# Kernel optimization log

Measured on AMD Instinct MI355X. Metric: run time of the kernel, lower is better.

Reference implementation:

```python
import jax, jax.numpy as jnp
import numpy as np

NQ, NH = 7, 4          # quantiles x horizons
G = NQ * NH            # 28 independent branches
IN_DIM, H1, H2 = 64, 64, 32


def setup_inputs() -> dict:
    key = jax.random.key(0)
    ks = jax.random.split(key, 7)
    B = 131072
    x = jax.random.normal(ks[0], (B, IN_DIM), dtype=jnp.float32)
    s1 = 1.0 / np.sqrt(IN_DIM)
    s2 = 1.0 / np.sqrt(H1)
    s3 = 1.0 / np.sqrt(H2)
    W1 = jax.random.uniform(ks[1], (G, IN_DIM, H1), jnp.float32, -s1, s1)
    b1 = jax.random.uniform(ks[2], (G, H1), jnp.float32, -s1, s1)
    W2 = jax.random.uniform(ks[3], (G, H1, H2), jnp.float32, -s2, s2)
    b2 = jax.random.uniform(ks[4], (G, H2), jnp.float32, -s2, s2)
    W3 = jax.random.uniform(ks[5], (G, H2, 1), jnp.float32, -s3, s3)
    b3 = jax.random.uniform(ks[6], (G, 1), jnp.float32, -s3, s3)
    return {"x": x, "W1": W1, "b1": b1, "W2": W2, "b2": b2, "W3": W3, "b3": b3}


def reference(x, W1, b1, W2, b2, W3, b3):
    # All G branches fused as batched GEMMs. x: [B, in]
    B = x.shape[0]
    h = jax.nn.relu(jnp.einsum('bi,gij->gbj', x, W1) + b1[:, None, :])   # [G,B,H1]
    h = jax.nn.relu(jnp.einsum('gbj,gjk->gbk', h, W2) + b2[:, None, :])  # [G,B,H2]
    o = jnp.einsum('gbk,gko->gbo', h, W3) + b3[:, None, :]               # [G,B,1]
    # branch order matches nested loop: quantile outer, horizon inner
    out = o[..., 0].reshape(NQ, NH, B).transpose(2, 0, 1)                # [B,NQ,NH]
    return out
```

## Files before the change

kernel.cpp:

```cpp
#include <hip/hip_runtime.h>
#include <hip/hip_bf16.h>
#include <hip/hip_fp16.h>

#define GN 28
#define G_TILE_BYTES 12288
#define WS_BYTES (GN * G_TILE_BYTES)

typedef __attribute__((ext_vector_type(4))) float f32x4;
typedef __attribute__((ext_vector_type(8))) short short8;
typedef _Float16 f16x8 __attribute__((ext_vector_type(8)));

__device__ __forceinline__ unsigned short f2h(float v){
  __half h = __float2half(v);
  return __builtin_bit_cast(unsigned short, h);
}
__device__ __forceinline__ f32x4 mfma16f(short8 a, short8 b, f32x4 c){
  return __builtin_amdgcn_mfma_f32_16x16x32_f16(
      __builtin_bit_cast(f16x8, a), __builtin_bit_cast(f16x8, b), c, 0, 0, 0);
}

__global__ void split_weights(const float* __restrict__ W1,
                              const float* __restrict__ W2,
                              unsigned char* __restrict__ ws){
  int t = blockIdx.x * 256 + threadIdx.x;
  if (t < 57344){
    int g = t >> 11, rem = t & 2047, n = rem >> 5, m = rem & 31;
    float v0 = W1[(g*64 + 2*m    )*64 + n];
    float v1 = W1[(g*64 + 2*m + 1)*64 + n];
    int off = (n*128 + 4*m) ^ ((n & 7) << 4);
    unsigned char* base = ws + g*G_TILE_BYTES;
    *(unsigned int*)(base + off) = (unsigned)f2h(v0) | ((unsigned)f2h(v1) << 16);
  } else {
    int t2 = t - 57344;
    int g = t2 >> 10, rem = t2 & 1023, n2 = rem >> 5, m = rem & 31;
    int kk = 2*m;
    int ks = kk >> 5, qq = (kk >> 3) & 3, u = (kk >> 2) & 1, i = kk & 3;
    int kn = 32*ks + 16*u + 4*qq + i;
    float v0 = W2[(g*64 + kn    )*32 + n2];
    float v1 = W2[(g*64 + kn + 1)*32 + n2];
    int off = (n2*128 + 4*m) ^ ((n2 & 7) << 4);
    unsigned char* base = ws + g*G_TILE_BYTES + 8192;
    *(unsigned int*)(base + off) = (unsigned)f2h(v0) | ((unsigned)f2h(v1) << 16);
  }
}

__global__ __launch_bounds__(256, 2) void mlp_fused(
    const float* __restrict__ x,  const float* __restrict__ b1,
    const float* __restrict__ b2, const float* __restrict__ W3,
    const float* __restrict__ b3, const unsigned char* __restrict__ ws,
    float* __restrict__ out){
  __shared__ uint4 wbuf[2][768];
  __shared__ float outb[256*28];
  __shared__ float biasL[3616];

  const int tid = threadIdx.x;
  const int wv  = tid >> 6;
  const int ln  = tid & 63;
  const int l15 = ln & 15;
  const int q   = ln >> 4;
  const int rowBase = blockIdx.x * 256 + wv * 64;

  #pragma unroll
  for (int i = 0; i < 7; ++i) biasL[i*256 + tid] = b1[i*256 + tid];
  if (tid < 128){
    #pragma unroll
    for (int i = 0; i < 7; ++i){
      biasL[1792 + i*128 + tid] = b2[i*128 + tid];
      biasL[2688 + i*128 + tid] = W3[i*128 + tid];
    }
  }
  if (tid < 28) biasL[3584 + tid] = b3[tid];

  short8 xf[4][2];
  #pragma unroll
  for (int rt = 0; rt < 4; ++rt)
    #pragma unroll
    for (int ks = 0; ks < 2; ++ks){
      const float* p = x + (rowBase + rt*16 + l15)*64 + ks*32 + q*8;
      f32x4 a = *(const f32x4*)p;
      f32x4 b = *(const f32x4*)(p + 4);
      short8 s;
      #pragma unroll
      for (int j = 0; j < 4; ++j){
        s[j]   = (short)f2h(a[j]);
        s[4+j] = (short)f2h(b[j]);
      }
      xf[rt][ks] = s;
    }

  auto stage = [&](int g, int buf){
    const unsigned char* gb = ws + g*G_TILE_BYTES + wv*3072 + ln*16;
    uint4* lb = &wbuf[buf][wv*192];
    #pragma unroll
    for (int it = 0; it < 3; ++it){
      __builtin_amdgcn_global_load_lds(
          (const __attribute__((address_space(1))) void*)(gb + it*1024),
          (__attribute__((address_space(3))) void*)(lb + it*64), 16, 0, 0);
    }
  };

  stage(0, 0);
  asm volatile("s_waitcnt vmcnt(0)" ::: "memory");
  __syncthreads();

  for (int g = 0; g < GN; ++g){
    const int cur = g & 1;
    if (g + 1 < GN) stage(g + 1, cur ^ 1);
    const uint4* wb = wbuf[cur];

    short8 a1[4][2];
    #pragma unroll
    for (int nt = 0; nt < 4; ++nt)
      #pragma unroll
      for (int ks = 0; ks < 2; ++ks){
        int n = nt*16 + l15;
        int off = ((n*128 + ks*64 + q*16) ^ ((n & 7) << 4)) >> 4;
        a1[nt][ks] = __builtin_bit_cast(short8, wb[off]);
      }
    f32x4 acc1[4][4];
    #pragma unroll
    for (int nt = 0; nt < 4; ++nt){
      f32x4 bias = *(const f32x4*)&biasL[g*64 + nt*16 + q*4];
      #pragma unroll
      for (int rt = 0; rt < 4; ++rt) acc1[nt][rt] = bias;
    }
    #pragma unroll
    for (int nt = 0; nt < 4; ++nt)
      #pragma unroll
      for (int rt = 0; rt < 4; ++rt)
        #pragma unroll
        for (int ks = 0; ks < 2; ++ks)
          acc1[nt][rt] = mfma16f(a1[nt][ks], xf[rt][ks], acc1[nt][rt]);

    short8 bh[4][2];
    #pragma unroll
    for (int rt = 0; rt < 4; ++rt)
      #pragma unroll
      for (int ks = 0; ks < 2; ++ks){
        f32x4 v0 = acc1[2*ks][rt], v1 = acc1[2*ks + 1][rt];
        short8 h;
        #pragma unroll
        for (int i = 0; i < 4; ++i){
          h[i]   = (short)f2h(fmaxf(v0[i], 0.0f));
          h[4+i] = (short)f2h(fmaxf(v1[i], 0.0f));
        }
        bh[rt][ks] = h;
      }

    short8 a2[2][2];
    #pragma unroll
    for (int nt = 0; nt < 2; ++nt)
      #pragma unroll
      for (int ks = 0; ks < 2; ++ks){
        int n2 = nt*16 + l15;
        int off = ((n2*128 + ks*64 + q*16) ^ ((n2 & 7) << 4)) >> 4;
        a2[nt][ks] = __builtin_bit_cast(short8, wb[512 + off]);
      }
    f32x4 acc2[2][4];
    #pragma unroll
    for (int nt = 0; nt < 2; ++nt){
      f32x4 bias = *(const f32x4*)&biasL[1792 + g*32 + nt*16 + q*4];
      #pragma unroll
      for (int rt = 0; rt < 4; ++rt) acc2[nt][rt] = bias;
    }
    #pragma unroll
    for (int nt = 0; nt < 2; ++nt)
      #pragma unroll
      for (int rt = 0; rt < 4; ++rt)
        #pragma unroll
        for (int ks = 0; ks < 2; ++ks)
          acc2[nt][rt] = mfma16f(a2[nt][ks], bh[rt][ks], acc2[nt][rt]);

    f32x4 w3f[2];
    #pragma unroll
    for (int nt = 0; nt < 2; ++nt)
      w3f[nt] = *(const f32x4*)&biasL[2688 + g*32 + nt*16 + q*4];
    float bias3 = biasL[3584 + g];
    #pragma unroll
    for (int rt = 0; rt < 4; ++rt){
      float p = 0.0f;
      #pragma unroll
      for (int nt = 0; nt < 2; ++nt)
        #pragma unroll
        for (int i = 0; i < 4; ++i)
          p = fmaf(fmaxf(acc2[nt][rt][i], 0.0f), w3f[nt][i], p);
      p += __shfl_xor(p, 16);
      p += __shfl_xor(p, 32);
      p += bias3;
      if (ln < 16)
        outb[(wv*64 + rt*16 + ln)*28 + g] = p;
    }

    asm volatile("s_waitcnt vmcnt(0)" ::: "memory");
    __syncthreads();
  }

  const int ob = blockIdx.x * (256*28);
  #pragma unroll
  for (int j = 0; j < 28; ++j){
    int idx = j*256 + tid;
    out[ob + idx] = outb[idx];
  }
}

extern "C" void kernel_launch(void* const* d_in, const int* in_sizes, int n_in,
                              void* d_out, int out_size, void* d_ws, size_t ws_size,
                              hipStream_t stream){
  const float* x  = (const float*)d_in[0];
  const float* W1 = (const float*)d_in[1];
  const float* b1 = (const float*)d_in[2];
  const float* W2 = (const float*)d_in[3];
  const float* b2 = (const float*)d_in[4];
  const float* W3 = (const float*)d_in[5];
  const float* b3 = (const float*)d_in[6];
  unsigned char* ws = (unsigned char*)d_ws;
  float* out = (float*)d_out;
  if (ws_size < (size_t)WS_BYTES) return;
  hipLaunchKernelGGL(split_weights, dim3(336), dim3(256), 0, stream, W1, W2, ws);
  hipLaunchKernelGGL(mlp_fused, dim3(512), dim3(256), 0, stream,
                     x, b1, b2, W3, b3, ws, out);
}
```

Baseline: 144.7 us.

## Halve rows per block, drop LDS output staging, rewrite weight prep with LDS transpose

The weight-prep kernel now runs one block per branch and transposes through LDS so that global reads and 16-byte writes are coalesced. The main kernel processes 128 rows per block instead of 256, doubling the grid, and allows up to 4 blocks per CU through launch bounds. The 28 KB output staging buffer is removed so that results are written straight to global memory. Biases are loaded once per branch and fed in as the MFMA initial accumulator. The intent is higher occupancy and less LDS pressure, at the cost of scattered 4-byte global output stores and reloading weight tiles for twice as many blocks.

```diff
diff --git a/kernel.cpp b/kernel.cpp
--- a/kernel.cpp
+++ b/kernel.cpp
@@ -19,38 +19,77 @@
       __builtin_bit_cast(f16x8, a), __builtin_bit_cast(f16x8, b), c, 0, 0, 0);
 }
 
-__global__ void split_weights(const float* __restrict__ W1,
-                              const float* __restrict__ W2,
-                              unsigned char* __restrict__ ws){
-  int t = blockIdx.x * 256 + threadIdx.x;
-  if (t < 57344){
-    int g = t >> 11, rem = t & 2047, n = rem >> 5, m = rem & 31;
-    float v0 = W1[(g*64 + 2*m    )*64 + n];
-    float v1 = W1[(g*64 + 2*m + 1)*64 + n];
-    int off = (n*128 + 4*m) ^ ((n & 7) << 4);
-    unsigned char* base = ws + g*G_TILE_BYTES;
-    *(unsigned int*)(base + off) = (unsigned)f2h(v0) | ((unsigned)f2h(v1) << 16);
-  } else {
-    int t2 = t - 57344;
-    int g = t2 >> 10, rem = t2 & 1023, n2 = rem >> 5, m = rem & 31;
-    int kk = 2*m;
-    int ks = kk >> 5, qq = (kk >> 3) & 3, u = (kk >> 2) & 1, i = kk & 3;
-    int kn = 32*ks + 16*u + 4*qq + i;
-    float v0 = W2[(g*64 + kn    )*32 + n2];
-    float v1 = W2[(g*64 + kn + 1)*32 + n2];
-    int off = (n2*128 + 4*m) ^ ((n2 & 7) << 4);
-    unsigned char* base = ws + g*G_TILE_BYTES + 8192;
-    *(unsigned int*)(base + off) = (unsigned)f2h(v0) | ((unsigned)f2h(v1) << 16);
-  }
-}
-
-__global__ __launch_bounds__(256, 2) void mlp_fused(
+__global__ __launch_bounds__(256) void prep_weights(
+    const float* __restrict__ W1, const float* __restrict__ W2,
+    unsigned char* __restrict__ ws){
+  __shared__ float t1[64*65];
+  __shared__ float t2[64*33];
+  const int g = blockIdx.x;
+  const int tid = threadIdx.x;
+
+  {
+    const f32x4* src = (const f32x4*)(W1 + g*4096);
+    int k = tid >> 2, n0 = (tid & 3) * 16;
+    #pragma unroll
+    for (int j = 0; j < 4; ++j){
+      f32x4 v = src[tid*4 + j];
+      #pragma unroll
+      for (int e = 0; e < 4; ++e) t1[k*65 + n0 + j*4 + e] = v[e];
+    }
+  }
+  {
+    const f32x4* src = (const f32x4*)(W2 + g*2048);
+    int k = tid >> 2, n0 = (tid & 3) * 8;
+    #pragma unroll
+    for (int j = 0; j < 2; ++j){
+      f32x4 v = src[tid*2 + j];
+      #pragma unroll
+      for (int e = 0; e < 4; ++e) t2[k*33 + n0 + j*4 + e] = v[e];
+    }
+  }
+  __syncthreads();
+
+  unsigned char* base = ws + g*G_TILE_BYTES;
+  {
+    int n = tid & 63, mh = tid >> 6;
+    #pragma unroll
+    for (int h = 0; h < 2; ++h){
+      unsigned w[4];
+      #pragma unroll
+      for (int mm = 0; mm < 4; ++mm){
+        int m = mh*8 + h*4 + mm;
+        float lo = t1[(2*m    )*65 + n];
+        float hi = t1[(2*m + 1)*65 + n];
+        w[mm] = (unsigned)f2h(lo) | ((unsigned)f2h(hi) << 16);
+      }
+      int off = (n*128 + mh*32 + h*16) ^ ((n & 7) << 4);
+      *(uint4*)(base + off) = make_uint4(w[0], w[1], w[2], w[3]);
+    }
+  }
+  {
+    int n2 = tid & 31, mq = tid >> 5;
+    unsigned w[4];
+    #pragma unroll
+    for (int mm = 0; mm < 4; ++mm){
+      int m = mq*4 + mm;
+      int kk = 2*m;
+      int ks = kk >> 5, qq = (kk >> 3) & 3, u = (kk >> 2) & 1, i = kk & 3;
+      int kn = 32*ks + 16*u + 4*qq + i;
+      float lo = t2[(kn    )*33 + n2];
+      float hi = t2[(kn + 1)*33 + n2];
+      w[mm] = (unsigned)f2h(lo) | ((unsigned)f2h(hi) << 16);
+    }
+    int off = (n2*128 + mq*16) ^ ((n2 & 7) << 4);
+    *(uint4*)(base + 8192 + off) = make_uint4(w[0], w[1], w[2], w[3]);
+  }
+}
+
+__global__ __launch_bounds__(256, 4) void mlp_fused(
     const float* __restrict__ x,  const float* __restrict__ b1,
     const float* __restrict__ b2, const float* __restrict__ W3,
     const float* __restrict__ b3, const unsigned char* __restrict__ ws,
     float* __restrict__ out){
   __shared__ uint4 wbuf[2][768];
-  __shared__ float outb[256*28];
   __shared__ float biasL[3616];
 
   const int tid = threadIdx.x;
@@ -58,22 +97,23 @@
   const int ln  = tid & 63;
   const int l15 = ln & 15;
   const int q   = ln >> 4;
-  const int rowBase = blockIdx.x * 256 + wv * 64;
+  const int rowBase = blockIdx.x * 128 + wv * 32;
 
   #pragma unroll
   for (int i = 0; i < 7; ++i) biasL[i*256 + tid] = b1[i*256 + tid];
-  if (tid < 128){
-    #pragma unroll
-    for (int i = 0; i < 7; ++i){
-      biasL[1792 + i*128 + tid] = b2[i*128 + tid];
-      biasL[2688 + i*128 + tid] = W3[i*128 + tid];
+  #pragma unroll
+  for (int i = 0; i < 4; ++i){
+    int idx = i*256 + tid;
+    if (idx < 896){
+      biasL[1792 + idx] = b2[idx];
+      biasL[2688 + idx] = W3[idx];
     }
   }
   if (tid < 28) biasL[3584 + tid] = b3[tid];
 
-  short8 xf[4][2];
+  short8 xf[2][2];
   #pragma unroll
-  for (int rt = 0; rt < 4; ++rt)
+  for (int rt = 0; rt < 2; ++rt)
     #pragma unroll
     for (int ks = 0; ks < 2; ++ks){
       const float* p = x + (rowBase + rt*16 + l15)*64 + ks*32 + q*8;
@@ -108,6 +148,17 @@
     if (g + 1 < GN) stage(g + 1, cur ^ 1);
     const uint4* wb = wbuf[cur];
 
+    f32x4 bias1[4], bias2[2], w3f[2];
+    #pragma unroll
+    for (int nt = 0; nt < 4; ++nt)
+      bias1[nt] = *(const f32x4*)&biasL[g*64 + nt*16 + q*4];
+    #pragma unroll
+    for (int nt = 0; nt < 2; ++nt){
+      bias2[nt] = *(const f32x4*)&biasL[1792 + g*32 + nt*16 + q*4];
+      w3f[nt]   = *(const f32x4*)&biasL[2688 + g*32 + nt*16 + q*4];
+    }
+    float bias3 = biasL[3584 + g];
+
     short8 a1[4][2];
     #pragma unroll
     for (int nt = 0; nt < 4; ++nt)
@@ -117,24 +168,18 @@
         int off = ((n*128 + ks*64 + q*16) ^ ((n & 7) << 4)) >> 4;
         a1[nt][ks] = __builtin_bit_cast(short8, wb[off]);
       }
-    f32x4 acc1[4][4];
-    #pragma unroll
-    for (int nt = 0; nt < 4; ++nt){
-      f32x4 bias = *(const f32x4*)&biasL[g*64 + nt*16 + q*4];
-      #pragma unroll
-      for (int rt = 0; rt < 4; ++rt) acc1[nt][rt] = bias;
-    }
+    f32x4 acc1[4][2];
     #pragma unroll
     for (int nt = 0; nt < 4; ++nt)
       #pragma unroll
-      for (int rt = 0; rt < 4; ++rt)
-        #pragma unroll
-        for (int ks = 0; ks < 2; ++ks)
-          acc1[nt][rt] = mfma16f(a1[nt][ks], xf[rt][ks], acc1[nt][rt]);
-
-    short8 bh[4][2];
-    #pragma unroll
-    for (int rt = 0; rt < 4; ++rt)
+      for (int rt = 0; rt < 2; ++rt){
+        acc1[nt][rt] = mfma16f(a1[nt][0], xf[rt][0], bias1[nt]);
+        acc1[nt][rt] = mfma16f(a1[nt][1], xf[rt][1], acc1[nt][rt]);
+      }
+
+    short8 bh[2][2];
+    #pragma unroll
+    for (int rt = 0; rt < 2; ++rt)
       #pragma unroll
       for (int ks = 0; ks < 2; ++ks){
         f32x4 v0 = acc1[2*ks][rt], v1 = acc1[2*ks + 1][rt];
@@ -156,28 +201,17 @@
         int off = ((n2*128 + ks*64 + q*16) ^ ((n2 & 7) << 4)) >> 4;
         a2[nt][ks] = __builtin_bit_cast(short8, wb[512 + off]);
       }
-    f32x4 acc2[2][4];
-    #pragma unroll
-    for (int nt = 0; nt < 2; ++nt){
-      f32x4 bias = *(const f32x4*)&biasL[1792 + g*32 + nt*16 + q*4];
-      #pragma unroll
-      for (int rt = 0; rt < 4; ++rt) acc2[nt][rt] = bias;
-    }
+    f32x4 acc2[2][2];
     #pragma unroll
     for (int nt = 0; nt < 2; ++nt)
       #pragma unroll
-      for (int rt = 0; rt < 4; ++rt)
-        #pragma unroll
-        for (int ks = 0; ks < 2; ++ks)
-          acc2[nt][rt] = mfma16f(a2[nt][ks], bh[rt][ks], acc2[nt][rt]);
-
-    f32x4 w3f[2];
-    #pragma unroll
-    for (int nt = 0; nt < 2; ++nt)
-      w3f[nt] = *(const f32x4*)&biasL[2688 + g*32 + nt*16 + q*4];
-    float bias3 = biasL[3584 + g];
-    #pragma unroll
-    for (int rt = 0; rt < 4; ++rt){
+      for (int rt = 0; rt < 2; ++rt){
+        acc2[nt][rt] = mfma16f(a2[nt][0], bh[rt][0], bias2[nt]);
+        acc2[nt][rt] = mfma16f(a2[nt][1], bh[rt][1], acc2[nt][rt]);
+      }
+
+    #pragma unroll
+    for (int rt = 0; rt < 2; ++rt){
       float p = 0.0f;
       #pragma unroll
       for (int nt = 0; nt < 2; ++nt)
@@ -188,18 +222,11 @@
       p += __shfl_xor(p, 32);
       p += bias3;
       if (ln < 16)
-        outb[(wv*64 + rt*16 + ln)*28 + g] = p;
+        out[(rowBase + rt*16 + ln)*28 + g] = p;
     }
 
     asm volatile("s_waitcnt vmcnt(0)" ::: "memory");
     __syncthreads();
-  }
-
-  const int ob = blockIdx.x * (256*28);
-  #pragma unroll
-  for (int j = 0; j < 28; ++j){
-    int idx = j*256 + tid;
-    out[ob + idx] = outb[idx];
   }
 }
 
@@ -216,7 +243,7 @@
   unsigned char* ws = (unsigned char*)d_ws;
   float* out = (float*)d_out;
   if (ws_size < (size_t)WS_BYTES) return;
-  hipLaunchKernelGGL(split_weights, dim3(336), dim3(256), 0, stream, W1, W2, ws);
-  hipLaunchKernelGGL(mlp_fused, dim3(512), dim3(256), 0, stream,
+  hipLaunchKernelGGL(prep_weights, dim3(GN), dim3(256), 0, stream, W1, W2, ws);
+  hipLaunchKernelGGL(mlp_fused, dim3(1024), dim3(256), 0, stream,
                      x, b1, b2, W3, b3, ws, out);
 }
```

Result: no change. 147.2 us (+1.8%).
